# Optimization experiments

Measured on AMD Instinct MI355X. Metric: run time of the kernel, lower is better.

## Reference

```python
import jax, jax.numpy as jnp
import numpy as np

N, M = 8192, 128
EPS = 1e-4


def setup_inputs() -> dict:
    key = jax.random.key(0)
    k1, k2, k3 = jax.random.split(key, 3)
    out1 = jax.random.normal(k1, (N, M), dtype=jnp.float32)
    out2 = jax.random.normal(k2, (N, M), dtype=jnp.float32)
    label = jax.random.uniform(k3, (N, N), dtype=jnp.float32)
    return {"out1": out1, "out2": out2, "label": label}


def _dir_loss(a, b, mob):
    # pairwise_inner_product(a, b) in the torch code equals b @ a.T:
    # inner[i, j] = <b[i], a[j]>
    scores = jnp.einsum('im,jm->ij', b, a)          # [n, n]
    phat = jax.nn.softmax(scores, axis=-1)
    return jnp.sum(-mob * jnp.log(phat + EPS))


def reference(out1, out2, label):
    loss = _dir_loss(out1, out2, label)
    loss = loss + _dir_loss(out2, out1, label.T)
    return loss
```

## Files before the change

kernel.cpp:

```cpp
#include <hip/hip_runtime.h>
#include <hip/hip_bf16.h>

#define NN 8192
#define MM 128
#define EPSF 1e-4f
#define SHIFT 30.0f

typedef __bf16 bf16x8 __attribute__((ext_vector_type(8)));
typedef __bf16 bf16x4 __attribute__((ext_vector_type(4)));
typedef float floatx4 __attribute__((ext_vector_type(4)));

__global__ void convert_kernel(const float* __restrict__ in0,
                               const float* __restrict__ in1,
                               __bf16* __restrict__ o0,
                               __bf16* __restrict__ o1) {
    const float* in = blockIdx.y ? in1 : in0;
    __bf16* out = blockIdx.y ? o1 : o0;
    int i = (blockIdx.x * blockDim.x + threadIdx.x) * 4;
    float4 v = *reinterpret_cast<const float4*>(in + i);
    bf16x4 o = { (__bf16)v.x, (__bf16)v.y, (__bf16)v.z, (__bf16)v.w };
    *reinterpret_cast<bf16x4*>(out + i) = o;
}

#define LOAD_A(dst, ptr)                                                   \
    do {                                                                   \
        dst[0] = *reinterpret_cast<const bf16x8*>((ptr) + 0);              \
        dst[1] = *reinterpret_cast<const bf16x8*>((ptr) + 32);             \
        dst[2] = *reinterpret_cast<const bf16x8*>((ptr) + 64);             \
        dst[3] = *reinterpret_cast<const bf16x8*>((ptr) + 96);             \
    } while (0)

__global__ __launch_bounds__(256)
void rowsum_kernel(const __bf16* __restrict__ X2, const __bf16* __restrict__ X1,
                   float* __restrict__ sums) {
    const int dir = blockIdx.z;
    const __bf16* A = dir ? X1 : X2;
    const __bf16* B = dir ? X2 : X1;
    float* sum = sums + dir * NN;

    const int tid = threadIdx.x;
    const int w = tid >> 6, lane = tid & 63, q = lane >> 4, ln = lane & 15;
    const int i0 = blockIdx.y * 128 + w * 32;
    const int jbase = blockIdx.x * 1024;

    bf16x8 a[2][4];
    #pragma unroll
    for (int rg = 0; rg < 2; ++rg) {
        const __bf16* ar = A + (size_t)(i0 + rg * 16 + ln) * MM + q * 8;
        LOAD_A(a[rg], ar);
    }

    float p[2][4] = {{0.f, 0.f, 0.f, 0.f}, {0.f, 0.f, 0.f, 0.f}};

    for (int js = 0; js < 16; ++js) {
        const int j0 = jbase + js * 64;
        #pragma unroll
        for (int cg = 0; cg < 4; ++cg) {
            const __bf16* br = B + (size_t)(j0 + cg * 16 + ln) * MM + q * 8;
            bf16x8 b[4];
            LOAD_A(b, br);
            floatx4 acc0 = {0.f, 0.f, 0.f, 0.f};
            floatx4 acc1 = {0.f, 0.f, 0.f, 0.f};
            #pragma unroll
            for (int k = 0; k < 4; ++k) {
                acc0 = __builtin_amdgcn_mfma_f32_16x16x32_bf16(a[0][k], b[k], acc0, 0, 0, 0);
                acc1 = __builtin_amdgcn_mfma_f32_16x16x32_bf16(a[1][k], b[k], acc1, 0, 0, 0);
            }
            #pragma unroll
            for (int r = 0; r < 4; ++r) {
                p[0][r] += __expf(acc0[r] - SHIFT);
                p[1][r] += __expf(acc1[r] - SHIFT);
            }
        }
    }

    #pragma unroll
    for (int m = 1; m <= 8; m <<= 1) {
        #pragma unroll
        for (int rg = 0; rg < 2; ++rg)
            #pragma unroll
            for (int r = 0; r < 4; ++r)
                p[rg][r] += __shfl_xor(p[rg][r], m);
    }
    if (ln == 0) {
        #pragma unroll
        for (int rg = 0; rg < 2; ++rg)
            #pragma unroll
            for (int r = 0; r < 4; ++r)
                atomicAdd(&sum[i0 + rg * 16 + q * 4 + r], p[rg][r]);
    }
}

__global__ void recip_kernel(const float* __restrict__ s, float* __restrict__ r) {
    int i = blockIdx.x * 256 + threadIdx.x;
    r[i] = 1.0f / s[i];
}

__global__ __launch_bounds__(256)
void loss_kernel(const __bf16* __restrict__ A, const __bf16* __restrict__ B,
                 const float* __restrict__ lrowR, const float* __restrict__ lcolR,
                 const float* __restrict__ label, float* __restrict__ out) {
    const int tid = threadIdx.x;
    const int w = tid >> 6, lane = tid & 63, q = lane >> 4, ln = lane & 15;
    const int i0 = blockIdx.y * 128 + w * 32;
    const int jbase = blockIdx.x * 256;

    bf16x8 a[2][4];
    float rlr[2][4];
    const float* labrow[2][4];
    #pragma unroll
    for (int rg = 0; rg < 2; ++rg) {
        const __bf16* ar = A + (size_t)(i0 + rg * 16 + ln) * MM + q * 8;
        LOAD_A(a[rg], ar);
        #pragma unroll
        for (int r = 0; r < 4; ++r) {
            const int row = i0 + rg * 16 + q * 4 + r;
            rlr[rg][r] = lrowR[row];
            labrow[rg][r] = label + (size_t)row * NN;
        }
    }

    float lacc = 0.f;
    for (int js = 0; js < 4; ++js) {
        const int j0 = jbase + js * 64;
        #pragma unroll
        for (int cg = 0; cg < 4; ++cg) {
            const int col = j0 + cg * 16 + ln;
            const __bf16* br = B + (size_t)col * MM + q * 8;
            bf16x8 b[4];
            LOAD_A(b, br);
            float rc = lcolR[col];
            float lb[2][4];
            #pragma unroll
            for (int rg = 0; rg < 2; ++rg)
                #pragma unroll
                for (int r = 0; r < 4; ++r) lb[rg][r] = labrow[rg][r][col];

            floatx4 acc0 = {0.f, 0.f, 0.f, 0.f};
            floatx4 acc1 = {0.f, 0.f, 0.f, 0.f};
            #pragma unroll
            for (int k = 0; k < 4; ++k) {
                acc0 = __builtin_amdgcn_mfma_f32_16x16x32_bf16(a[0][k], b[k], acc0, 0, 0, 0);
                acc1 = __builtin_amdgcn_mfma_f32_16x16x32_bf16(a[1][k], b[k], acc1, 0, 0, 0);
            }
            #pragma unroll
            for (int r = 0; r < 4; ++r) {
                float e0 = __expf(acc0[r] - SHIFT);
                float t0 = __logf(fmaf(e0, rlr[0][r], EPSF) * fmaf(e0, rc, EPSF));
                lacc = fmaf(lb[0][r], t0, lacc);
                float e1 = __expf(acc1[r] - SHIFT);
                float t1 = __logf(fmaf(e1, rlr[1][r], EPSF) * fmaf(e1, rc, EPSF));
                lacc = fmaf(lb[1][r], t1, lacc);
            }
        }
    }

    #pragma unroll
    for (int m = 1; m <= 32; m <<= 1) lacc += __shfl_xor(lacc, m);
    __shared__ float red[4];
    if (lane == 0) red[w] = lacc;
    __syncthreads();
    if (tid == 0) atomicAdd(out, -((red[0] + red[1]) + (red[2] + red[3])));
}

extern "C" void kernel_launch(void* const* d_in, const int* in_sizes, int n_in,
                              void* d_out, int out_size, void* d_ws, size_t ws_size,
                              hipStream_t stream) {
    const float* out1 = (const float*)d_in[0];
    const float* out2 = (const float*)d_in[1];
    const float* label = (const float*)d_in[2];

    char* ws = (char*)d_ws;
    __bf16* out1b = (__bf16*)ws;
    __bf16* out2b = (__bf16*)(ws + (size_t)(2 << 20));
    float* sums   = (float*)(ws + (size_t)(4 << 20));
    float* recips = sums + 2 * NN;

    hipMemsetAsync(sums, 0, 2 * NN * sizeof(float), stream);
    hipMemsetAsync(d_out, 0, sizeof(float), stream);

    convert_kernel<<<dim3(1024, 2), 256, 0, stream>>>(out1, out2, out1b, out2b);

    rowsum_kernel<<<dim3(8, 64, 2), 256, 0, stream>>>(out2b, out1b, sums);
    recip_kernel<<<dim3(64), 256, 0, stream>>>(sums, recips);

    loss_kernel<<<dim3(32, 64), 256, 0, stream>>>(out2b, out1b,
                                                  recips,
                                                  recips + NN,
                                                  label, (float*)d_out);
}
```

Before: 509.6 us.

## Transpose MFMA output layout in loss kernel for vectorized label loads; batch B loads

New measurement: 518.2 us. Within noise of the previous version (+1.7%).

```diff
diff --git a/kernel.cpp b/kernel.cpp
--- a/kernel.cpp
+++ b/kernel.cpp
@@ -54,17 +54,20 @@
 
     for (int js = 0; js < 16; ++js) {
         const int j0 = jbase + js * 64;
+        bf16x8 b[4][4];
         #pragma unroll
         for (int cg = 0; cg < 4; ++cg) {
             const __bf16* br = B + (size_t)(j0 + cg * 16 + ln) * MM + q * 8;
-            bf16x8 b[4];
-            LOAD_A(b, br);
+            LOAD_A(b[cg], br);
+        }
+        #pragma unroll
+        for (int cg = 0; cg < 4; ++cg) {
             floatx4 acc0 = {0.f, 0.f, 0.f, 0.f};
             floatx4 acc1 = {0.f, 0.f, 0.f, 0.f};
             #pragma unroll
             for (int k = 0; k < 4; ++k) {
-                acc0 = __builtin_amdgcn_mfma_f32_16x16x32_bf16(a[0][k], b[k], acc0, 0, 0, 0);
-                acc1 = __builtin_amdgcn_mfma_f32_16x16x32_bf16(a[1][k], b[k], acc1, 0, 0, 0);
+                acc0 = __builtin_amdgcn_mfma_f32_16x16x32_bf16(a[0][k], b[cg][k], acc0, 0, 0, 0);
+                acc1 = __builtin_amdgcn_mfma_f32_16x16x32_bf16(a[1][k], b[cg][k], acc1, 0, 0, 0);
             }
             #pragma unroll
             for (int r = 0; r < 4; ++r) {
@@ -106,51 +109,48 @@
     const int jbase = blockIdx.x * 256;
 
     bf16x8 a[2][4];
-    float rlr[2][4];
-    const float* labrow[2][4];
+    float rl[2];
+    const float* labp[2];
     #pragma unroll
     for (int rg = 0; rg < 2; ++rg) {
-        const __bf16* ar = A + (size_t)(i0 + rg * 16 + ln) * MM + q * 8;
-        LOAD_A(a[rg], ar);
-        #pragma unroll
-        for (int r = 0; r < 4; ++r) {
-            const int row = i0 + rg * 16 + q * 4 + r;
-            rlr[rg][r] = lrowR[row];
-            labrow[rg][r] = label + (size_t)row * NN;
-        }
+        const int row = i0 + rg * 16 + ln;
+        LOAD_A(a[rg], A + (size_t)row * MM + q * 8);
+        rl[rg] = lrowR[row];
+        labp[rg] = label + (size_t)row * NN;
     }
 
     float lacc = 0.f;
+    #pragma unroll
     for (int js = 0; js < 4; ++js) {
         const int j0 = jbase + js * 64;
+        floatx4 rc[4], lb[2][4];
         #pragma unroll
         for (int cg = 0; cg < 4; ++cg) {
-            const int col = j0 + cg * 16 + ln;
-            const __bf16* br = B + (size_t)col * MM + q * 8;
+            const int c4 = j0 + cg * 16 + q * 4;
+            rc[cg] = *reinterpret_cast<const floatx4*>(&lcolR[c4]);
+            lb[0][cg] = *reinterpret_cast<const floatx4*>(&labp[0][c4]);
+            lb[1][cg] = *reinterpret_cast<const floatx4*>(&labp[1][c4]);
+        }
+        #pragma unroll
+        for (int cg = 0; cg < 4; ++cg) {
+            const __bf16* br = B + (size_t)(j0 + cg * 16 + ln) * MM + q * 8;
             bf16x8 b[4];
             LOAD_A(b, br);
-            float rc = lcolR[col];
-            float lb[2][4];
-            #pragma unroll
-            for (int rg = 0; rg < 2; ++rg)
-                #pragma unroll
-                for (int r = 0; r < 4; ++r) lb[rg][r] = labrow[rg][r][col];
-
             floatx4 acc0 = {0.f, 0.f, 0.f, 0.f};
             floatx4 acc1 = {0.f, 0.f, 0.f, 0.f};
             #pragma unroll
             for (int k = 0; k < 4; ++k) {
-                acc0 = __builtin_amdgcn_mfma_f32_16x16x32_bf16(a[0][k], b[k], acc0, 0, 0, 0);
-                acc1 = __builtin_amdgcn_mfma_f32_16x16x32_bf16(a[1][k], b[k], acc1, 0, 0, 0);
+                acc0 = __builtin_amdgcn_mfma_f32_16x16x32_bf16(b[k], a[0][k], acc0, 0, 0, 0);
+                acc1 = __builtin_amdgcn_mfma_f32_16x16x32_bf16(b[k], a[1][k], acc1, 0, 0, 0);
             }
             #pragma unroll
             for (int r = 0; r < 4; ++r) {
                 float e0 = __expf(acc0[r] - SHIFT);
-                float t0 = __logf(fmaf(e0, rlr[0][r], EPSF) * fmaf(e0, rc, EPSF));
-                lacc = fmaf(lb[0][r], t0, lacc);
+                float t0 = __logf(fmaf(e0, rl[0], EPSF) * fmaf(e0, rc[cg][r], EPSF));
+                lacc = fmaf(lb[0][cg][r], t0, lacc);
                 float e1 = __expf(acc1[r] - SHIFT);
-                float t1 = __logf(fmaf(e1, rlr[1][r], EPSF) * fmaf(e1, rc, EPSF));
-                lacc = fmaf(lb[1][r], t1, lacc);
+                float t1 = __logf(fmaf(e1, rl[1], EPSF) * fmaf(e1, rc[cg][r], EPSF));
+                lacc = fmaf(lb[1][cg][r], t1, lacc);
             }
         }
     }
```
